# Kernel tuning notes

Measured on AMD Instinct MI355X. Metric: run time of the kernel, lower is better.

Reference implementation:

```python
import jax, jax.numpy as jnp
import numpy as np

NUM_STEPS = 5


def setup_inputs() -> dict:
    key = jax.random.key(0)
    ks = jax.random.split(key, 12)
    B, N, H, E, A = 8, 1024, 64, 2, 8
    initial_state = jax.random.normal(ks[0], (B, N, H), dtype=jnp.float32)
    annotation = jax.random.normal(ks[1], (B, N, A), dtype=jnp.float32)
    # sparse-ish positive adjacency, scaled so matmul outputs don't saturate gates
    adj_matrix = jax.random.uniform(ks[2], (B, N, 2 * N * E), dtype=jnp.float32) * 0.01
    s = 0.05
    W_edge = jax.random.normal(ks[3], (H, H * E), dtype=jnp.float32) * s
    b_edge = jax.random.normal(ks[4], (H * E,), dtype=jnp.float32) * s
    W_gate = jax.random.normal(ks[5], (3 * H, H), dtype=jnp.float32) * s
    b_gate = jax.random.normal(ks[6], (H,), dtype=jnp.float32) * s
    W_hid = jax.random.normal(ks[7], (H + A, H), dtype=jnp.float32) * s
    b_hid = jax.random.normal(ks[8], (H,), dtype=jnp.float32) * s
    W_out = jax.random.normal(ks[9], (H, 1), dtype=jnp.float32) * s
    b_out = jax.random.normal(ks[10], (1,), dtype=jnp.float32) * s
    return dict(initial_state=initial_state, annotation=annotation, adj_matrix=adj_matrix,
                W_edge=W_edge, b_edge=b_edge, W_gate=W_gate, b_gate=b_gate,
                W_hid=W_hid, b_hid=b_hid, W_out=W_out, b_out=b_out)


def reference(initial_state, annotation, adj_matrix, W_edge, b_edge,
              W_gate, b_gate, W_hid, b_hid, W_out, b_out):
    B, N, H = initial_state.shape
    E = W_edge.shape[1] // H
    boundary = N * E
    A_in = adj_matrix[:, :, :boundary]   # [B, N, N*E]
    A_out = adj_matrix[:, :, boundary:]  # [B, N, N*E]

    h = initial_state
    for _ in range(NUM_STEPS):
        # Linear(H, H*E) then view/transpose to [B, N*E, H].
        # Original computes incoming_edge and outgoing_edge with the SAME
        # linear on the SAME input -> identical tensors; compute once.
        edge = jnp.einsum('bnh,he->bne', h, W_edge) + b_edge      # [B, N, H*E]
        edge = edge.reshape(B, N, H, E).transpose(0, 3, 1, 2).reshape(B, N * E, H)
        a_in = jnp.matmul(A_in, edge)    # [B, N, H]
        a_out = jnp.matmul(A_out, edge)  # [B, N, H]
        a = jnp.concatenate([a_in, a_out, h], axis=2)             # [B, N, 3H]
        # update and reset use the same gate linear -> equal; compute once.
        z = jax.nn.sigmoid(jnp.einsum('bnk,kh->bnh', a, W_gate) + b_gate)
        a_r = jnp.concatenate([a_in, a_out, z * h], axis=2)
        h_tilde = jnp.tanh(jnp.einsum('bnk,kh->bnh', a_r, W_gate) + b_gate)
        h = (1.0 - z) * h + z * h_tilde

    # task_id not in {18, 19}: node-level output head
    ha = jnp.concatenate([h, annotation], axis=2)                 # [B, N, H+A]
    out = jnp.tanh(jnp.einsum('bnk,kh->bnh', ha, W_hid) + b_hid)  # [B, N, H]
    out = (jnp.einsum('bnh,ho->bno', out, W_out) + b_out).sum(axis=2)  # [B, N]
    return out
```

## Files before the change

### kernel.cpp

```cpp
#include <hip/hip_runtime.h>
#include <math.h>

#define BN    8
#define NN    1024
#define HH    64
#define ADIM  8
#define STEPS 5
#define K2    2048
#define ROWS  (BN*NN)

typedef __attribute__((ext_vector_type(8))) short bf16x8;
typedef __attribute__((ext_vector_type(4))) float f32x4;

__device__ __forceinline__ unsigned short f2bf(float f) {
    unsigned int u = __float_as_uint(f);
    u += 0x7FFF + ((u >> 16) & 1);
    return (unsigned short)(u >> 16);
}
__device__ __forceinline__ float bf2f(unsigned short h) {
    return __uint_as_float(((unsigned int)h) << 16);
}

__device__ __forceinline__ void lgkm_barrier() {
    asm volatile("s_waitcnt lgkmcnt(0)" ::: "memory");
    __builtin_amdgcn_s_barrier();
    asm volatile("" ::: "memory");
}

__global__ __launch_bounds__(256) void conv_adj(
    const float* __restrict__ in, unsigned short* __restrict__ out)
{
    int tid = blockIdx.x * 256 + threadIdx.x;
    #pragma unroll
    for (int i = 0; i < 4; ++i) {
        size_t idx = (size_t)tid + (size_t)i * 2097152;
        float4 v = ((const float4*)in)[idx];
        ushort4 o;
        o.x = f2bf(v.x); o.y = f2bf(v.y); o.z = f2bf(v.z); o.w = f2bf(v.w);
        ((ushort4*)out)[idx] = o;
    }
}

__global__ __launch_bounds__(256) void prep_pack(
    const float* __restrict__ Wg, const float* __restrict__ We,
    unsigned short* __restrict__ wgp, unsigned short* __restrict__ wep)
{
    int t = blockIdx.x * 256 + threadIdx.x;
    if (t < 12288) {
        int k = t >> 6, c = t & 63;
        float v = Wg[t];
        unsigned short hi = f2bf(v);
        unsigned short lo = f2bf(v - bf2f(hi));
        wgp[(size_t)c * 192 + k] = hi;
        wgp[(size_t)(64 + c) * 192 + k] = lo;
    } else if (t < 20480) {
        int u = t - 12288;
        int k = u >> 7, c = u & 127;
        float v = We[u];
        unsigned short hi = f2bf(v);
        unsigned short lo = f2bf(v - bf2f(hi));
        wep[(size_t)c * 64 + k] = hi;
        wep[(size_t)(128 + c) * 64 + k] = lo;
    }
}

__global__ __launch_bounds__(256) void init_kernel(
    const float* __restrict__ init_state,
    const float* __restrict__ We, const float* __restrict__ be,
    float* __restrict__ h_ws, unsigned short* __restrict__ edge_t)
{
    __shared__ float h_lds[4][65];
    int t = threadIdx.x;
    int r = t >> 6, hp = t & 63;
    int row = blockIdx.x * 4 + r;
    float hv = init_state[(size_t)row * 64 + hp];
    h_ws[(size_t)row * 64 + hp] = hv;
    h_lds[r][hp] = hv;
    __syncthreads();
    int b = row >> 10, n = row & 1023;
    #pragma unroll
    for (int e = 0; e < 2; ++e) {
        float acc = be[hp * 2 + e];
        #pragma unroll 8
        for (int c = 0; c < 64; ++c)
            acc += h_lds[r][c] * We[c * 128 + hp * 2 + e];
        edge_t[((size_t)b * 64 + hp) * K2 + e * NN + n] = f2bf(acc);
    }
}

__global__ __launch_bounds__(512) void step_kernel(
    const unsigned short* __restrict__ adjb,
    const unsigned short* __restrict__ ein,
    unsigned short* __restrict__ eout,
    float* __restrict__ h_ws,
    const unsigned short* __restrict__ wgp,
    const unsigned short* __restrict__ wep,
    const float* __restrict__ bg,
    const float* __restrict__ be,
    int do_edge)
{
    __shared__ __attribute__((aligned(16))) unsigned short Bs[2][64][264];
    __shared__ __attribute__((aligned(16))) unsigned short Xhi[32][200];
    __shared__ __attribute__((aligned(16))) unsigned short Xlo[32][200];
    __shared__ __attribute__((aligned(16))) float          hf [32][68];
    __shared__ __attribute__((aligned(16))) unsigned short HNhi[32][72];
    __shared__ __attribute__((aligned(16))) unsigned short HNlo[32][72];

    int t  = threadIdx.x;
    int b  = blockIdx.x >> 5;
    int mt = blockIdx.x & 31;
    int n0 = mt * 32;
    size_t hbase = ((size_t)(b * NN + n0)) * 64;

    int lane = t & 63, w = t >> 6, l15 = lane & 15, q = lane >> 4;
    int dir = w >> 2, rh = (w >> 1) & 1, kc = w & 1;

    const unsigned short* Abase = adjb
        + ((size_t)(b * NN + n0 + rh * 16 + l15)) * 4096 + dir * K2 + kc * 128;

    int srow[4], scol[4];
    const unsigned short* sptr[4];
    #pragma unroll
    for (int i = 0; i < 4; ++i) {
        int u = i * 512 + t;
        srow[i] = u >> 5; scol[i] = (u & 31) * 8;
        sptr[i] = ein + ((size_t)b * 64 + srow[i]) * K2 + scol[i];
    }

    int hr = t >> 4, hcg = (t & 15) * 4;
    float4 hv4 = *(const float4*)(h_ws + hbase + (size_t)hr * 64 + hcg);

    uint4 gA[4], gB[4];
    #pragma unroll
    for (int i = 0; i < 4; ++i) gA[i] = *(const uint4*)(sptr[i]);
    #pragma unroll
    for (int i = 0; i < 4; ++i) gB[i] = *(const uint4*)(sptr[i] + 256);
    bf16x8 afA[4], afB[4];
    #pragma unroll
    for (int ks = 0; ks < 4; ++ks)
        afA[ks] = *(const bf16x8*)(Abase + ks * 32 + q * 8);
    #pragma unroll
    for (int ks = 0; ks < 4; ++ks)
        afB[ks] = *(const bf16x8*)(Abase + 256 + ks * 32 + q * 8);

    {
        float vv[4] = {hv4.x, hv4.y, hv4.z, hv4.w};
        #pragma unroll
        for (int j = 0; j < 4; ++j) {
            float hv = vv[j];
            unsigned short hi = f2bf(hv), lo = f2bf(hv - bf2f(hi));
            Xhi[hr][128 + hcg + j] = hi;
            Xlo[hr][128 + hcg + j] = lo;
            hf[hr][hcg + j] = hv;
        }
    }

    #pragma unroll
    for (int i = 0; i < 4; ++i)
        *(uint4*)&Bs[0][srow[i]][scol[i]] = gA[i];
    lgkm_barrier();

    f32x4 acc[4];
    #pragma unroll
    for (int ct = 0; ct < 4; ++ct) acc[ct] = (f32x4){0.f, 0.f, 0.f, 0.f};

    #pragma unroll
    for (int c = 0; c < 8; ++c) {
        const int par = c & 1;
        if (c < 6) {
            #pragma unroll
            for (int i = 0; i < 4; ++i) {
                uint4 v = *(const uint4*)(sptr[i] + (c + 2) * 256);
                if (par == 0) gA[i] = v; else gB[i] = v;
            }
        }
        #pragma unroll
        for (int ks = 0; ks < 4; ++ks) {
            bf16x8 a = (par == 0) ? afA[ks] : afB[ks];
            #pragma unroll
            for (int ct = 0; ct < 4; ++ct) {
                bf16x8 bfr = *(const bf16x8*)&Bs[par][ct * 16 + l15][kc * 128 + ks * 32 + q * 8];
                acc[ct] = __builtin_amdgcn_mfma_f32_16x16x32_bf16(a, bfr, acc[ct], 0, 0, 0);
            }
        }
        if (c < 6) {
            #pragma unroll
            for (int ks = 0; ks < 4; ++ks) {
                bf16x8 v = *(const bf16x8*)(Abase + (c + 2) * 256 + ks * 32 + q * 8);
                if (par == 0) afA[ks] = v; else afB[ks] = v;
            }
        }
        if (c < 7) {
            #pragma unroll
            for (int i = 0; i < 4; ++i) {
                uint4 v = (par == 0) ? gB[i] : gA[i];
                *(uint4*)&Bs[par ^ 1][srow[i]][scol[i]] = v;
            }
        }
        lgkm_barrier();
    }

    float (*red)[16][68] = (float (*)[16][68])(&Bs[0][0][0]);
    int gg = w >> 1;
    if (kc == 1) {
        #pragma unroll
        for (int ct = 0; ct < 4; ++ct)
            #pragma unroll
            for (int i = 0; i < 4; ++i)
                red[gg][q * 4 + i][ct * 16 + l15] = acc[ct][i];
    }
    __syncthreads();
    if (kc == 0) {
        #pragma unroll
        for (int ct = 0; ct < 4; ++ct)
            #pragma unroll
            for (int i = 0; i < 4; ++i) {
                float v = acc[ct][i] + red[gg][q * 4 + i][ct * 16 + l15];
                unsigned short hi = f2bf(v), lo = f2bf(v - bf2f(hi));
                int r  = rh * 16 + q * 4 + i;
                int cc2 = dir * 64 + ct * 16 + l15;
                Xhi[r][cc2] = hi;
                Xlo[r][cc2] = lo;
            }
    }
    __syncthreads();

    int mg = w & 1, cg16 = w >> 1;
    int arow = mg * 16 + l15;
    int cc = cg16 * 16 + l15;
    const unsigned short* wcol = wgp + (size_t)cc * 192;
    f32x4 as = (f32x4){0.f, 0.f, 0.f, 0.f}, az;

    #pragma unroll
    for (int ks = 0; ks < 4; ++ks) {
        bf16x8 ah = *(const bf16x8*)&Xhi[arow][ks * 32 + q * 8];
        bf16x8 al = *(const bf16x8*)&Xlo[arow][ks * 32 + q * 8];
        const unsigned short* wb = wcol + ks * 32 + q * 8;
        bf16x8 bh = *(const bf16x8*)wb;
        bf16x8 bl = *(const bf16x8*)(wb + 64 * 192);
        as = __builtin_amdgcn_mfma_f32_16x16x32_bf16(ah, bh, as, 0, 0, 0);
        as = __builtin_amdgcn_mfma_f32_16x16x32_bf16(ah, bl, as, 0, 0, 0);
        as = __builtin_amdgcn_mfma_f32_16x16x32_bf16(al, bh, as, 0, 0, 0);
    }
    az = as;
    #pragma unroll
    for (int ks = 4; ks < 6; ++ks) {
        bf16x8 ah = *(const bf16x8*)&Xhi[arow][ks * 32 + q * 8];
        bf16x8 al = *(const bf16x8*)&Xlo[arow][ks * 32 + q * 8];
        const unsigned short* wb = wcol + ks * 32 + q * 8;
        bf16x8 bh = *(const bf16x8*)wb;
        bf16x8 bl = *(const bf16x8*)(wb + 64 * 192);
        az = __builtin_amdgcn_mfma_f32_16x16x32_bf16(ah, bh, az, 0, 0, 0);
        az = __builtin_amdgcn_mfma_f32_16x16x32_bf16(ah, bl, az, 0, 0, 0);
        az = __builtin_amdgcn_mfma_f32_16x16x32_bf16(al, bh, az, 0, 0, 0);
    }
    __syncthreads();

    float zv[4], hv[4];
    float bgv = bg[cc];
    #pragma unroll
    for (int i = 0; i < 4; ++i) {
        int r = mg * 16 + q * 4 + i;
        float z = 1.f / (1.f + __expf(-(az[i] + bgv)));
        float h = hf[r][cc];
        zv[i] = z; hv[i] = h;
        float zh = z * h;
        unsigned short hi = f2bf(zh), lo = f2bf(zh - bf2f(hi));
        Xhi[r][128 + cc] = hi;
        Xlo[r][128 + cc] = lo;
    }
    __syncthreads();

    #pragma unroll
    for (int ks = 4; ks < 6; ++ks) {
        bf16x8 ah = *(const bf16x8*)&Xhi[arow][ks * 32 + q * 8];
        bf16x8 al = *(const bf16x8*)&Xlo[arow][ks * 32 + q * 8];
        const unsigned short* wb = wcol + ks * 32 + q * 8;
        bf16x8 bh = *(const bf16x8*)wb;
        bf16x8 bl = *(const bf16x8*)(wb + 64 * 192);
        as = __builtin_amdgcn_mfma_f32_16x16x32_bf16(ah, bh, as, 0, 0, 0);
        as = __builtin_amdgcn_mfma_f32_16x16x32_bf16(ah, bl, as, 0, 0, 0);
        as = __builtin_amdgcn_mfma_f32_16x16x32_bf16(al, bh, as, 0, 0, 0);
    }

    #pragma unroll
    for (int i = 0; i < 4; ++i) {
        int r = mg * 16 + q * 4 + i;
        float ht = tanhf(as[i] + bgv);
        float z  = zv[i];
        float hn = (1.f - z) * hv[i] + z * ht;
        h_ws[hbase + (size_t)r * 64 + cc] = hn;
        if (do_edge) {
            unsigned short hi = f2bf(hn), lo = f2bf(hn - bf2f(hi));
            HNhi[r][cc] = hi;
            HNlo[r][cc] = lo;
        }
    }
    if (!do_edge) return;
    __syncthreads();

    int me = w & 1, cb2 = (w >> 1) * 2;
    int erow = me * 16 + l15;
    f32x4 ae[2];
    ae[0] = ae[1] = (f32x4){0.f, 0.f, 0.f, 0.f};
    #pragma unroll
    for (int ks = 0; ks < 2; ++ks) {
        bf16x8 ah = *(const bf16x8*)&HNhi[erow][ks * 32 + q * 8];
        bf16x8 al = *(const bf16x8*)&HNlo[erow][ks * 32 + q * 8];
        #pragma unroll
        for (int p = 0; p < 2; ++p) {
            int ec = (cb2 + p) * 16 + l15;
            const unsigned short* wb = wep + (size_t)ec * 64 + ks * 32 + q * 8;
            bf16x8 bh = *(const bf16x8*)wb;
            bf16x8 bl = *(const bf16x8*)(wb + 128 * 64);
            ae[p] = __builtin_amdgcn_mfma_f32_16x16x32_bf16(ah, bh, ae[p], 0, 0, 0);
            ae[p] = __builtin_amdgcn_mfma_f32_16x16x32_bf16(ah, bl, ae[p], 0, 0, 0);
            ae[p] = __builtin_amdgcn_mfma_f32_16x16x32_bf16(al, bh, ae[p], 0, 0, 0);
        }
    }
    #pragma unroll
    for (int p = 0; p < 2; ++p) {
        int ec = (cb2 + p) * 16 + l15;
        float bev = be[ec];
        int hp2 = ec >> 1, e = ec & 1;
        size_t ebase = ((size_t)b * 64 + hp2) * K2 + (size_t)e * NN
                     + n0 + me * 16 + q * 4;
        ushort4 ev;
        ev.x = f2bf(ae[p][0] + bev);
        ev.y = f2bf(ae[p][1] + bev);
        ev.z = f2bf(ae[p][2] + bev);
        ev.w = f2bf(ae[p][3] + bev);
        *(ushort4*)(eout + ebase) = ev;
    }
}

__global__ __launch_bounds__(256) void head_kernel(
    const float* __restrict__ h_ws, const float* __restrict__ ann,
    const float* __restrict__ Wh, const float* __restrict__ bh,
    const float* __restrict__ Wo, const float* __restrict__ bo,
    float* __restrict__ out)
{
    __shared__ float Wh_l[72 * 64];
    __shared__ float ha[4][72];
    int t = threadIdx.x;
    #pragma unroll
    for (int l = 0; l < 18; ++l) {
        int idx = t + l * 256;
        Wh_l[idx] = Wh[idx];
    }
    int r = t >> 6, hp = t & 63;
    int row = blockIdx.x * 4 + r;
    ha[r][hp] = h_ws[(size_t)row * 64 + hp];
    if (hp < ADIM) ha[r][64 + hp] = ann[(size_t)row * ADIM + hp];
    __syncthreads();

    float acc = bh[hp];
    #pragma unroll 8
    for (int k = 0; k < 72; ++k)
        acc += ha[r][k] * Wh_l[k * 64 + hp];
    float v = tanhf(acc) * Wo[hp];
    #pragma unroll
    for (int o = 32; o; o >>= 1) v += __shfl_down(v, o, 64);
    if (hp == 0) out[row] = v + bo[0];
}

extern "C" void kernel_launch(void* const* d_in, const int* in_sizes, int n_in,
                              void* d_out, int out_size, void* d_ws, size_t ws_size,
                              hipStream_t stream) {
    const float* init_state = (const float*)d_in[0];
    const float* ann = (const float*)d_in[1];
    const float* adj = (const float*)d_in[2];
    const float* We  = (const float*)d_in[3];
    const float* be  = (const float*)d_in[4];
    const float* Wg  = (const float*)d_in[5];
    const float* bg  = (const float*)d_in[6];
    const float* Wh  = (const float*)d_in[7];
    const float* bh  = (const float*)d_in[8];
    const float* Wo  = (const float*)d_in[9];
    const float* bo  = (const float*)d_in[10];
    float* out = (float*)d_out;

    char* wsb = (char*)d_ws;
    unsigned short* adjb   = (unsigned short*)wsb;
    unsigned short* edge_a = (unsigned short*)(wsb + 67108864);
    unsigned short* edge_b = (unsigned short*)(wsb + 69206016);
    float*          h_ws   = (float*)(wsb + 71303168);
    unsigned short* wgp    = (unsigned short*)(wsb + 73400320);
    unsigned short* wep    = (unsigned short*)(wsb + 73449472);

    conv_adj<<<dim3(8192), dim3(256), 0, stream>>>(adj, adjb);
    prep_pack<<<dim3(80), dim3(256), 0, stream>>>(Wg, We, wgp, wep);
    init_kernel<<<dim3(ROWS / 4), dim3(256), 0, stream>>>(init_state, We, be, h_ws, edge_a);
    for (int s = 0; s < STEPS; ++s) {
        const unsigned short* ein = (s & 1) ? edge_b : edge_a;
        unsigned short* eo        = (s & 1) ? edge_a : edge_b;
        step_kernel<<<dim3(256), dim3(512), 0, stream>>>(
            adjb, ein, eo, h_ws, wgp, wep, bg, be, (s < STEPS - 1) ? 1 : 0);
    }
    head_kernel<<<dim3(ROWS / 4), dim3(256), 0, stream>>>(h_ws, ann, Wh, bh, Wo, bo, out);
}
```

Measured before the change: 381.6 us.

## Tile adjacency into MFMA fragment layout and fuse output head into last step

The bf16 conversion of the adjacency matrix now writes it in a tiled layout, so each wave's A-fragment loads become contiguous 512-element chunks instead of strided row reads. The output head is folded into the final step kernel, using LDS-resident h, which removes a separate launch and the h round-trip. tanhf is replaced by an exp-based fast tanh. The tiled conversion adds an LDS transpose stage, and the fast tanh can lose some accuracy for large arguments.

```diff
diff --git a/kernel.cpp b/kernel.cpp
--- a/kernel.cpp
+++ b/kernel.cpp
@@ -20,6 +20,10 @@
 __device__ __forceinline__ float bf2f(unsigned short h) {
     return __uint_as_float(((unsigned int)h) << 16);
 }
+__device__ __forceinline__ float ftanh(float x) {
+    float e = __expf(2.f * x);
+    return 1.f - 2.f / (e + 1.f);
+}
 
 __device__ __forceinline__ void lgkm_barrier() {
     asm volatile("s_waitcnt lgkmcnt(0)" ::: "memory");
@@ -27,17 +31,38 @@
     asm volatile("" ::: "memory");
 }
 
+
 __global__ __launch_bounds__(256) void conv_adj(
     const float* __restrict__ in, unsigned short* __restrict__ out)
 {
-    int tid = blockIdx.x * 256 + threadIdx.x;
-    #pragma unroll
-    for (int i = 0; i < 4; ++i) {
-        size_t idx = (size_t)tid + (size_t)i * 2097152;
-        float4 v = ((const float4*)in)[idx];
+    __shared__ unsigned short tl[8][520];
+    int bid = blockIdx.x;
+    int kg = bid & 7;
+    int ng = (bid >> 3) & 63;
+    int d  = (bid >> 9) & 1;
+    int b  = bid >> 10;
+    int t = threadIdx.x;
+
+    const float* src = in + ((size_t)(b * 1024 + ng * 16)) * 4096 + d * 2048 + kg * 256;
+    #pragma unroll
+    for (int it = 0; it < 4; ++it) {
+        int u = it * 256 + t;
+        int r = u >> 6, c4 = u & 63;
+        float4 v = *(const float4*)(src + (size_t)r * 4096 + c4 * 4);
+        int k = c4 * 4;
+        int kb = k >> 5, kk = k & 31;
         ushort4 o;
         o.x = f2bf(v.x); o.y = f2bf(v.y); o.z = f2bf(v.z); o.w = f2bf(v.w);
-        ((ushort4*)out)[idx] = o;
+        *(ushort4*)&tl[kb][r * 32 + kk] = o;
+    }
+    __syncthreads();
+
+    unsigned short* dst = out + (((size_t)(b * 2 + d) * 64 + kg * 8) * 64 + ng) * 512;
+    #pragma unroll
+    for (int it = 0; it < 4; ++it) {
+        int u = it * 256 + t;
+        int kb = u >> 7, wo = u & 127;
+        *(ushort4*)(dst + (size_t)kb * 32768 + wo * 4) = *(const ushort4*)&tl[kb][wo * 4];
     }
 }
 
@@ -89,7 +114,7 @@
 }
 
 __global__ __launch_bounds__(512) void step_kernel(
-    const unsigned short* __restrict__ adjb,
+    const unsigned short* __restrict__ adjf,
     const unsigned short* __restrict__ ein,
     unsigned short* __restrict__ eout,
     float* __restrict__ h_ws,
@@ -97,7 +122,11 @@
     const unsigned short* __restrict__ wep,
     const float* __restrict__ bg,
     const float* __restrict__ be,
-    int do_edge)
+    const float* __restrict__ ann,
+    const float* __restrict__ Wh, const float* __restrict__ bh,
+    const float* __restrict__ Wo, const float* __restrict__ bo,
+    float* __restrict__ out,
+    int mode)
 {
     __shared__ __attribute__((aligned(16))) unsigned short Bs[2][64][264];
     __shared__ __attribute__((aligned(16))) unsigned short Xhi[32][200];
@@ -114,9 +143,10 @@
 
     int lane = t & 63, w = t >> 6, l15 = lane & 15, q = lane >> 4;
     int dir = w >> 2, rh = (w >> 1) & 1, kc = w & 1;
-
-    const unsigned short* Abase = adjb
-        + ((size_t)(b * NN + n0 + rh * 16 + l15)) * 4096 + dir * K2 + kc * 128;
+    int nb  = mt * 2 + rh;
+
+    const unsigned short* A2 = adjf
+        + (((size_t)(b * 2 + dir) * 64 + kc * 4) * 64 + nb) * 512 + l15 * 32 + q * 8;
 
     int srow[4], scol[4];
     const unsigned short* sptr[4];
@@ -138,10 +168,10 @@
     bf16x8 afA[4], afB[4];
     #pragma unroll
     for (int ks = 0; ks < 4; ++ks)
-        afA[ks] = *(const bf16x8*)(Abase + ks * 32 + q * 8);
+        afA[ks] = *(const bf16x8*)(A2 + (size_t)ks * 32768);
     #pragma unroll
     for (int ks = 0; ks < 4; ++ks)
-        afB[ks] = *(const bf16x8*)(Abase + 256 + ks * 32 + q * 8);
+        afB[ks] = *(const bf16x8*)(A2 + (size_t)(8 + ks) * 32768);
 
     {
         float vv[4] = {hv4.x, hv4.y, hv4.z, hv4.w};
@@ -186,7 +216,7 @@
         if (c < 6) {
             #pragma unroll
             for (int ks = 0; ks < 4; ++ks) {
-                bf16x8 v = *(const bf16x8*)(Abase + (c + 2) * 256 + ks * 32 + q * 8);
+                bf16x8 v = *(const bf16x8*)(A2 + (size_t)((c + 2) * 8 + ks) * 32768);
                 if (par == 0) afA[ks] = v; else afB[ks] = v;
             }
         }
@@ -236,11 +266,11 @@
         bf16x8 ah = *(const bf16x8*)&Xhi[arow][ks * 32 + q * 8];
         bf16x8 al = *(const bf16x8*)&Xlo[arow][ks * 32 + q * 8];
         const unsigned short* wb = wcol + ks * 32 + q * 8;
-        bf16x8 bh = *(const bf16x8*)wb;
-        bf16x8 bl = *(const bf16x8*)(wb + 64 * 192);
-        as = __builtin_amdgcn_mfma_f32_16x16x32_bf16(ah, bh, as, 0, 0, 0);
-        as = __builtin_amdgcn_mfma_f32_16x16x32_bf16(ah, bl, as, 0, 0, 0);
-        as = __builtin_amdgcn_mfma_f32_16x16x32_bf16(al, bh, as, 0, 0, 0);
+        bf16x8 bh2 = *(const bf16x8*)wb;
+        bf16x8 bl2 = *(const bf16x8*)(wb + 64 * 192);
+        as = __builtin_amdgcn_mfma_f32_16x16x32_bf16(ah, bh2, as, 0, 0, 0);
+        as = __builtin_amdgcn_mfma_f32_16x16x32_bf16(ah, bl2, as, 0, 0, 0);
+        as = __builtin_amdgcn_mfma_f32_16x16x32_bf16(al, bh2, as, 0, 0, 0);
     }
     az = as;
     #pragma unroll
@@ -248,11 +278,11 @@
         bf16x8 ah = *(const bf16x8*)&Xhi[arow][ks * 32 + q * 8];
         bf16x8 al = *(const bf16x8*)&Xlo[arow][ks * 32 + q * 8];
         const unsigned short* wb = wcol + ks * 32 + q * 8;
-        bf16x8 bh = *(const bf16x8*)wb;
-        bf16x8 bl = *(const bf16x8*)(wb + 64 * 192);
-        az = __builtin_amdgcn_mfma_f32_16x16x32_bf16(ah, bh, az, 0, 0, 0);
-        az = __builtin_amdgcn_mfma_f32_16x16x32_bf16(ah, bl, az, 0, 0, 0);
-        az = __builtin_amdgcn_mfma_f32_16x16x32_bf16(al, bh, az, 0, 0, 0);
+        bf16x8 bh2 = *(const bf16x8*)wb;
+        bf16x8 bl2 = *(const bf16x8*)(wb + 64 * 192);
+        az = __builtin_amdgcn_mfma_f32_16x16x32_bf16(ah, bh2, az, 0, 0, 0);
+        az = __builtin_amdgcn_mfma_f32_16x16x32_bf16(ah, bl2, az, 0, 0, 0);
+        az = __builtin_amdgcn_mfma_f32_16x16x32_bf16(al, bh2, az, 0, 0, 0);
     }
     __syncthreads();
 
@@ -276,92 +306,94 @@
         bf16x8 ah = *(const bf16x8*)&Xhi[arow][ks * 32 + q * 8];
         bf16x8 al = *(const bf16x8*)&Xlo[arow][ks * 32 + q * 8];
         const unsigned short* wb = wcol + ks * 32 + q * 8;
-        bf16x8 bh = *(const bf16x8*)wb;
-        bf16x8 bl = *(const bf16x8*)(wb + 64 * 192);
-        as = __builtin_amdgcn_mfma_f32_16x16x32_bf16(ah, bh, as, 0, 0, 0);
-        as = __builtin_amdgcn_mfma_f32_16x16x32_bf16(ah, bl, as, 0, 0, 0);
-        as = __builtin_amdgcn_mfma_f32_16x16x32_bf16(al, bh, as, 0, 0, 0);
+        bf16x8 bh2 = *(const bf16x8*)wb;
+        bf16x8 bl2 = *(const bf16x8*)(wb + 64 * 192);
+        as = __builtin_amdgcn_mfma_f32_16x16x32_bf16(ah, bh2, as, 0, 0, 0);
+        as = __builtin_amdgcn_mfma_f32_16x16x32_bf16(ah, bl2, as, 0, 0, 0);
+        as = __builtin_amdgcn_mfma_f32_16x16x32_bf16(al, bh2, as, 0, 0, 0);
     }
 
     #pragma unroll
     for (int i = 0; i < 4; ++i) {
         int r = mg * 16 + q * 4 + i;
-        float ht = tanhf(as[i] + bgv);
+        float ht = ftanh(as[i] + bgv);
         float z  = zv[i];
         float hn = (1.f - z) * hv[i] + z * ht;
-        h_ws[hbase + (size_t)r * 64 + cc] = hn;
-        if (do_edge) {
+        if (mode == 0) {
+            h_ws[hbase + (size_t)r * 64 + cc] = hn;
             unsigned short hi = f2bf(hn), lo = f2bf(hn - bf2f(hi));
             HNhi[r][cc] = hi;
             HNlo[r][cc] = lo;
-        }
-    }
-    if (!do_edge) return;
-    __syncthreads();
-
-    int me = w & 1, cb2 = (w >> 1) * 2;
-    int erow = me * 16 + l15;
-    f32x4 ae[2];
-    ae[0] = ae[1] = (f32x4){0.f, 0.f, 0.f, 0.f};
-    #pragma unroll
-    for (int ks = 0; ks < 2; ++ks) {
-        bf16x8 ah = *(const bf16x8*)&HNhi[erow][ks * 32 + q * 8];
-        bf16x8 al = *(const bf16x8*)&HNlo[erow][ks * 32 + q * 8];
+        } else {
+            hf[r][cc] = hn;
+        }
+    }
+    __syncthreads();
+
+    if (mode == 0) {
+        int me = w & 1, cb2 = (w >> 1) * 2;
+        int erow = me * 16 + l15;
+        f32x4 ae[2];
+        ae[0] = ae[1] = (f32x4){0.f, 0.f, 0.f, 0.f};
+        #pragma unroll
+        for (int ks = 0; ks < 2; ++ks) {
+            bf16x8 ah = *(const bf16x8*)&HNhi[erow][ks * 32 + q * 8];
+            bf16x8 al = *(const bf16x8*)&HNlo[erow][ks * 32 + q * 8];
+            #pragma unroll
+            for (int p = 0; p < 2; ++p) {
+                int ec = (cb2 + p) * 16 + l15;
+                const unsigned short* wb = wep + (size_t)ec * 64 + ks * 32 + q * 8;
+                bf16x8 bh2 = *(const bf16x8*)wb;
+                bf16x8 bl2 = *(const bf16x8*)(wb + 128 * 64);
+                ae[p] = __builtin_amdgcn_mfma_f32_16x16x32_bf16(ah, bh2, ae[p], 0, 0, 0);
+                ae[p] = __builtin_amdgcn_mfma_f32_16x16x32_bf16(ah, bl2, ae[p], 0, 0, 0);
+                ae[p] = __builtin_amdgcn_mfma_f32_16x16x32_bf16(al, bh2, ae[p], 0, 0, 0);
+            }
+        }
         #pragma unroll
         for (int p = 0; p < 2; ++p) {
             int ec = (cb2 + p) * 16 + l15;
-            const unsigned short* wb = wep + (size_t)ec * 64 + ks * 32 + q * 8;
-            bf16x8 bh = *(const bf16x8*)wb;
-            bf16x8 bl = *(const bf16x8*)(wb + 128 * 64);
-            ae[p] = __builtin_amdgcn_mfma_f32_16x16x32_bf16(ah, bh, ae[p], 0, 0, 0);
-            ae[p] = __builtin_amdgcn_mfma_f32_16x16x32_bf16(ah, bl, ae[p], 0, 0, 0);
-            ae[p] = __builtin_amdgcn_mfma_f32_16x16x32_bf16(al, bh, ae[p], 0, 0, 0);
-        }
-    }
-    #pragma unroll
-    for (int p = 0; p < 2; ++p) {
-        int ec = (cb2 + p) * 16 + l15;
-        float bev = be[ec];
-        int hp2 = ec >> 1, e = ec & 1;
-        size_t ebase = ((size_t)b * 64 + hp2) * K2 + (size_t)e * NN
-                     + n0 + me * 16 + q * 4;
-        ushort4 ev;
-        ev.x = f2bf(ae[p][0] + bev);
-        ev.y = f2bf(ae[p][1] + bev);
-        ev.z = f2bf(ae[p][2] + bev);
-        ev.w = f2bf(ae[p][3] + bev);
-        *(ushort4*)(eout + ebase) = ev;
-    }
-}
-
-__global__ __launch_bounds__(256) void head_kernel(
-    const float* __restrict__ h_ws, const float* __restrict__ ann,
-    const float* __restrict__ Wh, const float* __restrict__ bh,
-    const float* __restrict__ Wo, const float* __restrict__ bo,
-    float* __restrict__ out)
-{
-    __shared__ float Wh_l[72 * 64];
-    __shared__ float ha[4][72];
-    int t = threadIdx.x;
-    #pragma unroll
-    for (int l = 0; l < 18; ++l) {
-        int idx = t + l * 256;
-        Wh_l[idx] = Wh[idx];
-    }
-    int r = t >> 6, hp = t & 63;
-    int row = blockIdx.x * 4 + r;
-    ha[r][hp] = h_ws[(size_t)row * 64 + hp];
-    if (hp < ADIM) ha[r][64 + hp] = ann[(size_t)row * ADIM + hp];
-    __syncthreads();
-
-    float acc = bh[hp];
-    #pragma unroll 8
-    for (int k = 0; k < 72; ++k)
-        acc += ha[r][k] * Wh_l[k * 64 + hp];
-    float v = tanhf(acc) * Wo[hp];
-    #pragma unroll
-    for (int o = 32; o; o >>= 1) v += __shfl_down(v, o, 64);
-    if (hp == 0) out[row] = v + bo[0];
+            float bev = be[ec];
+            int hp2 = ec >> 1, e = ec & 1;
+            size_t ebase = ((size_t)b * 64 + hp2) * K2 + (size_t)e * NN
+                         + n0 + me * 16 + q * 4;
+            ushort4 ev;
+            ev.x = f2bf(ae[p][0] + bev);
+            ev.y = f2bf(ae[p][1] + bev);
+            ev.z = f2bf(ae[p][2] + bev);
+            ev.w = f2bf(ae[p][3] + bev);
+            *(ushort4*)(eout + ebase) = ev;
+        }
+    } else {
+        int r = t >> 4, hq = (t & 15) * 4;
+        int row = b * NN + n0 + r;
+        float av[ADIM];
+        #pragma unroll
+        for (int j = 0; j < ADIM; ++j) av[j] = ann[(size_t)row * ADIM + j];
+        float ac2[4];
+        #pragma unroll
+        for (int i = 0; i < 4; ++i) ac2[i] = bh[hq + i];
+        #pragma unroll 8
+        for (int k = 0; k < 64; ++k) {
+            float hv2 = hf[r][k];
+            float4 wv = *(const float4*)&Wh[k * 64 + hq];
+            ac2[0] += hv2 * wv.x; ac2[1] += hv2 * wv.y;
+            ac2[2] += hv2 * wv.z; ac2[3] += hv2 * wv.w;
+        }
+        #pragma unroll
+        for (int k = 0; k < ADIM; ++k) {
+            float4 wv = *(const float4*)&Wh[(64 + k) * 64 + hq];
+            ac2[0] += av[k] * wv.x; ac2[1] += av[k] * wv.y;
+            ac2[2] += av[k] * wv.z; ac2[3] += av[k] * wv.w;
+        }
+        float v = 0.f;
+        #pragma unroll
+        for (int i = 0; i < 4; ++i)
+            v += ftanh(ac2[i]) * Wo[hq + i];
+        #pragma unroll
+        for (int m = 8; m; m >>= 1) v += __shfl_xor(v, m, 64);
+        if ((t & 15) == 0) out[row] = v + bo[0];
+    }
 }
 
 extern "C" void kernel_launch(void* const* d_in, const int* in_sizes, int n_in,
@@ -381,21 +413,21 @@
     float* out = (float*)d_out;
 
     char* wsb = (char*)d_ws;
-    unsigned short* adjb   = (unsigned short*)wsb;
+    unsigned short* adjf   = (unsigned short*)wsb;
     unsigned short* edge_a = (unsigned short*)(wsb + 67108864);
     unsigned short* edge_b = (unsigned short*)(wsb + 69206016);
     float*          h_ws   = (float*)(wsb + 71303168);
     unsigned short* wgp    = (unsigned short*)(wsb + 73400320);
     unsigned short* wep    = (unsigned short*)(wsb + 73449472);
 
-    conv_adj<<<dim3(8192), dim3(256), 0, stream>>>(adj, adjb);
+    conv_adj<<<dim3(8192), dim3(256), 0, stream>>>(adj, adjf);
     prep_pack<<<dim3(80), dim3(256), 0, stream>>>(Wg, We, wgp, wep);
     init_kernel<<<dim3(ROWS / 4), dim3(256), 0, stream>>>(init_state, We, be, h_ws, edge_a);
     for (int s = 0; s < STEPS; ++s) {
         const unsigned short* ein = (s & 1) ? edge_b : edge_a;
         unsigned short* eo        = (s & 1) ? edge_a : edge_b;
         step_kernel<<<dim3(256), dim3(512), 0, stream>>>(
-            adjb, ein, eo, h_ws, wgp, wep, bg, be, (s < STEPS - 1) ? 1 : 0);
-    }
-    head_kernel<<<dim3(ROWS / 4), dim3(256), 0, stream>>>(h_ws, ann, Wh, bh, Wo, bo, out);
-}
+            adjf, ein, eo, h_ws, wgp, wep, bg, be,
+            ann, Wh, bh, Wo, bo, out, (s == STEPS - 1) ? 1 : 0);
+    }
+}
```

Result: no change. 377.4 us (-1.1%).
